# Performance work log

Measured on AMD Instinct MI355X. Metric: run time of the kernel, lower is better.

Reference implementation:

```python
import jax, jax.numpy as jnp
import numpy as np

N_NODES = 50000
N_EDGES = 800000
IN_CH, HID_CH, OUT_CH = 128, 128, 64


def _glorot(key, out_c, in_c):
    lim = (6.0 / (in_c + out_c)) ** 0.5
    return jax.random.uniform(key, (out_c, in_c), jnp.float32, -lim, lim)


def setup_inputs() -> dict:
    key = jax.random.key(0)
    ks = jax.random.split(key, 12)
    x = jax.random.normal(ks[0], (N_NODES, IN_CH), jnp.float32)
    edge_index = jax.random.randint(ks[1], (2, N_EDGES), 0, N_NODES, dtype=jnp.int64)
    # 4 SAGEConv layers: 128->128, 128->128, 128->64, 64->64
    dims = [(IN_CH, HID_CH), (HID_CH, HID_CH), (HID_CH, OUT_CH), (OUT_CH, OUT_CH)]
    params = {}
    for i, (ci, co) in enumerate(dims, start=1):
        params[f"Wl{i}"] = _glorot(ks[2 * i], co, ci)          # neighbor (aggregated) transform
        params[f"bl{i}"] = jnp.zeros((co,), jnp.float32)
        params[f"Wr{i}"] = _glorot(ks[2 * i + 1], co, ci)      # root/self transform (no bias in PyG)
    return {"x": x, "edge_index": edge_index, **params}


def _sage_conv(x, src, dst, Wl, bl, Wr):
    # mean aggregation of source features at destination nodes
    msgs = x[src]                                                   # [E, C] gather
    summed = jax.ops.segment_sum(msgs, dst, num_segments=N_NODES)   # [N, C] scatter-add
    cnt = jax.ops.segment_sum(jnp.ones((src.shape[0], 1), x.dtype), dst, num_segments=N_NODES)
    mean = summed / jnp.maximum(cnt, 1.0)
    return mean @ Wl.T + bl + x @ Wr.T


def reference(x, edge_index, Wl1, bl1, Wr1, Wl2, bl2, Wr2, Wl3, bl3, Wr3, Wl4, bl4, Wr4):
    src, dst = edge_index[0], edge_index[1]
    # conv1 = GraphSAGE(in, hid, num_layers=2): relu between layers only
    h = jax.nn.relu(_sage_conv(x, src, dst, Wl1, bl1, Wr1))
    h = _sage_conv(h, src, dst, Wl2, bl2, Wr2)
    h = jax.nn.relu(h)  # model-level .relu()
    # conv2 = GraphSAGE(hid, out, num_layers=2)
    h = jax.nn.relu(_sage_conv(h, src, dst, Wl3, bl3, Wr3))
    h = _sage_conv(h, src, dst, Wl4, bl4, Wr4)
    return jax.nn.log_softmax(h, axis=1)
```

## Files before the change

### kernel.cpp

```cpp
#include <hip/hip_runtime.h>
#include <hip/hip_bf16.h>


typedef __attribute__((ext_vector_type(8))) short bf16x8;
typedef __attribute__((ext_vector_type(4))) float f32x4;

#define NBKT 512
#define BSHIFT 7
#define BCAP 3072
#define EPB 2048

__device__ __forceinline__ unsigned short f2bf(float f) {
    __hip_bfloat16 h = __float2bfloat16(f);
    return __builtin_bit_cast(unsigned short, h);
}
__device__ __forceinline__ float bflo(unsigned int u) {
    return __builtin_bit_cast(float, u << 16);
}
__device__ __forceinline__ float bfhi(unsigned int u) {
    return __builtin_bit_cast(float, u & 0xffff0000u);
}

__global__ void zero_ints(int* __restrict__ p, int n) {
    int i = blockIdx.x * blockDim.x + threadIdx.x;
    if (i < n) p[i] = 0;
}

__global__ __launch_bounds__(256) void wconv(
    const float* __restrict__ s0, const float* __restrict__ s1,
    const float* __restrict__ s2, const float* __restrict__ s3,
    const float* __restrict__ s4, const float* __restrict__ s5,
    const float* __restrict__ s6, const float* __restrict__ s7,
    unsigned short* __restrict__ wb)
{
    const int b = blockIdx.x;
    const float* src;
    int seg_blk, dst_off;
    if      (b < 16) { src = s0; seg_blk = b;      dst_off = 0; }
    else if (b < 32) { src = s1; seg_blk = b - 16; dst_off = 16384; }
    else if (b < 48) { src = s2; seg_blk = b - 32; dst_off = 32768; }
    else if (b < 64) { src = s3; seg_blk = b - 48; dst_off = 49152; }
    else if (b < 72) { src = s4; seg_blk = b - 64; dst_off = 65536; }
    else if (b < 80) { src = s5; seg_blk = b - 72; dst_off = 73728; }
    else if (b < 84) { src = s6; seg_blk = b - 80; dst_off = 81920; }
    else             { src = s7; seg_blk = b - 84; dst_off = 86016; }
    int i = seg_blk * 1024 + threadIdx.x * 4;
    float4 v = *reinterpret_cast<const float4*>(src + i);
    ushort4 o = {f2bf(v.x), f2bf(v.y), f2bf(v.z), f2bf(v.w)};
    *reinterpret_cast<ushort4*>(wb + dst_off + i) = o;
}

__global__ __launch_bounds__(256) void partition_edges(
    const int* __restrict__ ei, int E,
    int* __restrict__ gcur, unsigned int* __restrict__ ppk)
{
    __shared__ int hist[NBKT];
    __shared__ int base[NBKT];
    const int tid = threadIdx.x;
    for (int i = tid; i < NBKT; i += 256) hist[i] = 0;
    __syncthreads();

    const int e0 = blockIdx.x * EPB;
    int bket[8], rank[8];
    unsigned int pk[8];
    #pragma unroll
    for (int k = 0; k < 8; ++k) {
        int e = e0 + k * 256 + tid;
        bket[k] = -1;
        if (e < E) {
            int d = ei[E + e], s = ei[e];
            int b = d >> BSHIFT;
            bket[k] = b;
            pk[k] = ((unsigned int)(d & ((1 << BSHIFT) - 1)) << 16) | (unsigned int)s;
            rank[k] = atomicAdd(&hist[b], 1);
        }
    }
    __syncthreads();
    for (int i = tid; i < NBKT; i += 256)
        base[i] = hist[i] ? atomicAdd(&gcur[i], hist[i]) : 0;
    __syncthreads();
    #pragma unroll
    for (int k = 0; k < 8; ++k) {
        if (bket[k] >= 0) {
            int off = base[bket[k]] + rank[k];
            if (off < BCAP)
                ppk[(size_t)bket[k] * BCAP + off] = pk[k];
        }
    }
}

__global__ __launch_bounds__(512) void scan_gcur(
    const int* __restrict__ gcur, int* __restrict__ bbase,
    int* __restrict__ offs, int N)
{
    const int tid = threadIdx.x;
    int v = min(gcur[tid], BCAP);
    int x = v;
    #pragma unroll
    for (int d = 1; d < 64; d <<= 1) {
        int t = __shfl_up(x, d);
        if ((tid & 63) >= d) x += t;
    }
    __shared__ int ws[8];
    if ((tid & 63) == 63) ws[tid >> 6] = x;
    __syncthreads();
    int add = 0;
    for (int w = 0; w < (tid >> 6); ++w) add += ws[w];
    int incl = x + add;
    bbase[tid] = incl - v;
    if (tid == 511) offs[N] = incl;
}

__global__ __launch_bounds__(256) void bucket_sort(
    const unsigned int* __restrict__ ppk, const int* __restrict__ gcur,
    const int* __restrict__ bbase,
    int* __restrict__ offs, int* __restrict__ srcs, int N)
{
    const int b = blockIdx.x;
    const int n = min(gcur[b], BCAP);
    const int bb = bbase[b];
    const int tid = threadIdx.x;

    __shared__ unsigned int eL[BCAP];
    __shared__ int cnt[1 << BSHIFT], excl[1 << BSHIFT], cur[1 << BSHIFT];

    if (tid < (1 << BSHIFT)) cnt[tid] = 0;
    for (int i = tid; i < n; i += 256) eL[i] = ppk[(size_t)b * BCAP + i];
    __syncthreads();
    for (int i = tid; i < n; i += 256) atomicAdd(&cnt[eL[i] >> 16], 1);
    __syncthreads();

    int v = 0, x = 0;
    if (tid < 128) {
        v = cnt[tid];
        x = v;
        #pragma unroll
        for (int d = 1; d < 64; d <<= 1) {
            int t = __shfl_up(x, d);
            if ((tid & 63) >= d) x += t;
        }
    }
    __shared__ int w0;
    if (tid == 63) w0 = x;
    __syncthreads();
    if (tid < 128) {
        int incl = x + ((tid >= 64) ? w0 : 0);
        excl[tid] = incl - v;
        cur[tid] = incl - v;
    }
    __syncthreads();

    for (int i = tid; i < n; i += 256) {
        unsigned int pk = eL[i];
        int d = (int)(pk >> 16);
        int pos = atomicAdd(&cur[d], 1);
        srcs[bb + pos] = (int)(pk & 0xffffu);
    }
    if (tid < 128) {
        int gn = (b << BSHIFT) + tid;
        if (gn < N) offs[gn] = bb + excl[tid];
    }
}

template <int K, int Cout, int ZBF, int F32IN>
__global__ __launch_bounds__(256) void gemm_yz_mfma(
    const void* __restrict__ Hv,
    const unsigned short* __restrict__ Wlb, const unsigned short* __restrict__ Wrb,
    unsigned short* __restrict__ Y, unsigned short* __restrict__ Zb,
    float* __restrict__ Zf, int N)
{
    constexpr int BM = 128, BN = 128;
    constexpr int ROWH = K + 8;
    __shared__ unsigned short Hs[BM * ROWH];
    __shared__ unsigned short Ws[BN * ROWH];

    const int tid = threadIdx.x;
    const int bm = blockIdx.x * BM;
    const int bn = blockIdx.y * BN;

    if (F32IN) {
        const float* H = (const float*)Hv;
        constexpr int C4 = K / 4;
        for (int c = tid; c < BM * C4; c += 256) {
            int row = c / C4, k4 = (c % C4) * 4;
            int grow = bm + row;
            float4 vv = make_float4(0.f, 0.f, 0.f, 0.f);
            if (grow < N) vv = *reinterpret_cast<const float4*>(&H[(size_t)grow * K + k4]);
            ushort4 o = {f2bf(vv.x), f2bf(vv.y), f2bf(vv.z), f2bf(vv.w)};
            *reinterpret_cast<ushort4*>(&Hs[row * ROWH + k4]) = o;
        }
    } else {
        const unsigned short* H = (const unsigned short*)Hv;
        constexpr int C8 = K / 8;
        for (int c = tid; c < BM * C8; c += 256) {
            int row = c / C8, k8 = (c % C8) * 8;
            int grow = bm + row;
            int4 vv = {0, 0, 0, 0};
            if (grow < N) vv = *reinterpret_cast<const int4*>(&H[(size_t)grow * K + k8]);
            *reinterpret_cast<int4*>(&Hs[row * ROWH + k8]) = vv;
        }
    }
    {
        constexpr int C8 = K / 8;
        for (int c = tid; c < BN * C8; c += 256) {
            int row = c / C8, k8 = (c % C8) * 8;
            int gcol = bn + row;
            const unsigned short* wsrc = (gcol < Cout) ? (Wlb + (size_t)gcol * K)
                                                       : (Wrb + (size_t)(gcol - Cout) * K);
            int4 vv = *reinterpret_cast<const int4*>(wsrc + k8);
            *reinterpret_cast<int4*>(&Ws[row * ROWH + k8]) = vv;
        }
    }
    __syncthreads();

    const int wid = tid >> 6, lane = tid & 63;
    const int wr = wid >> 1, wc = wid & 1;
    const int l15 = lane & 15, lhi = lane >> 4;

    f32x4 acc[4][4] = {};
    #pragma unroll
    for (int k0 = 0; k0 < K; k0 += 32) {
        const int colOff = k0 + lhi * 8;
        bf16x8 a[4], bfr[4];
        #pragma unroll
        for (int m = 0; m < 4; ++m)
            a[m] = *reinterpret_cast<const bf16x8*>(&Hs[(wr * 64 + m * 16 + l15) * ROWH + colOff]);
        #pragma unroll
        for (int nn = 0; nn < 4; ++nn)
            bfr[nn] = *reinterpret_cast<const bf16x8*>(&Ws[(wc * 64 + nn * 16 + l15) * ROWH + colOff]);
        #pragma unroll
        for (int m = 0; m < 4; ++m)
            #pragma unroll
            for (int nn = 0; nn < 4; ++nn)
                acc[m][nn] = __builtin_amdgcn_mfma_f32_16x16x32_bf16(a[m], bfr[nn], acc[m][nn], 0, 0, 0);
    }

    #pragma unroll
    for (int m = 0; m < 4; ++m) {
        #pragma unroll
        for (int nn = 0; nn < 4; ++nn) {
            int gcol = bn + wc * 64 + nn * 16 + l15;
            #pragma unroll
            for (int j = 0; j < 4; ++j) {
                int grow = bm + wr * 64 + m * 16 + lhi * 4 + j;
                if (grow < N) {
                    if (gcol < Cout)      Y[(size_t)grow * Cout + gcol] = f2bf(acc[m][nn][j]);
                    else if (ZBF)         Zb[(size_t)grow * Cout + (gcol - Cout)] = f2bf(acc[m][nn][j]);
                    else                  Zf[(size_t)grow * Cout + (gcol - Cout)] = acc[m][nn][j];
                }
            }
        }
    }
}

__global__ __launch_bounds__(256) void agg128_bf(
    const unsigned short* __restrict__ Y, const unsigned short* __restrict__ Zb,
    const float* __restrict__ bl,
    const int* __restrict__ offs, const int* __restrict__ srcs,
    unsigned short* __restrict__ OUT, int N)
{
    const int node = blockIdx.x * 4 + (threadIdx.x >> 6);
    if (node >= N) return;
    const int lane = threadIdx.x & 63;
    const int h = lane >> 5, l31 = lane & 31;
    const int beg = offs[node], end = offs[node + 1];

    float a0 = 0.f, a1 = 0.f, a2 = 0.f, a3 = 0.f;
    int e = beg + h;
    for (; e + 6 < end; e += 8) {
        int s0 = srcs[e], s1 = srcs[e + 2], s2 = srcs[e + 4], s3 = srcs[e + 6];
        uint2 u0 = *reinterpret_cast<const uint2*>(&Y[(size_t)s0 * 128 + 4 * l31]);
        uint2 u1 = *reinterpret_cast<const uint2*>(&Y[(size_t)s1 * 128 + 4 * l31]);
        uint2 u2 = *reinterpret_cast<const uint2*>(&Y[(size_t)s2 * 128 + 4 * l31]);
        uint2 u3 = *reinterpret_cast<const uint2*>(&Y[(size_t)s3 * 128 + 4 * l31]);
        a0 += bflo(u0.x) + bflo(u1.x) + bflo(u2.x) + bflo(u3.x);
        a1 += bfhi(u0.x) + bfhi(u1.x) + bfhi(u2.x) + bfhi(u3.x);
        a2 += bflo(u0.y) + bflo(u1.y) + bflo(u2.y) + bflo(u3.y);
        a3 += bfhi(u0.y) + bfhi(u1.y) + bfhi(u2.y) + bfhi(u3.y);
    }
    for (; e < end; e += 2) {
        uint2 u = *reinterpret_cast<const uint2*>(&Y[(size_t)srcs[e] * 128 + 4 * l31]);
        a0 += bflo(u.x); a1 += bfhi(u.x); a2 += bflo(u.y); a3 += bfhi(u.y);
    }
    a0 += __shfl_xor(a0, 32);
    a1 += __shfl_xor(a1, 32);
    a2 += __shfl_xor(a2, 32);
    a3 += __shfl_xor(a3, 32);

    if (h == 0) {
        float inv = 1.0f / fmaxf((float)(end - beg), 1.0f);
        uint2 zu = *reinterpret_cast<const uint2*>(&Zb[(size_t)node * 128 + 4 * l31]);
        float4 bb = *reinterpret_cast<const float4*>(&bl[4 * l31]);
        float o0 = fmaxf(a0 * inv + bflo(zu.x) + bb.x, 0.f);
        float o1 = fmaxf(a1 * inv + bfhi(zu.x) + bb.y, 0.f);
        float o2 = fmaxf(a2 * inv + bflo(zu.y) + bb.z, 0.f);
        float o3 = fmaxf(a3 * inv + bfhi(zu.y) + bb.w, 0.f);
        uint2 pk;
        pk.x = (unsigned int)f2bf(o0) | ((unsigned int)f2bf(o1) << 16);
        pk.y = (unsigned int)f2bf(o2) | ((unsigned int)f2bf(o3) << 16);
        *reinterpret_cast<uint2*>(&OUT[(size_t)node * 128 + 4 * l31]) = pk;
    }
}

__global__ __launch_bounds__(256) void agg64_mid(
    const unsigned short* __restrict__ Y, const unsigned short* __restrict__ Zb,
    const float* __restrict__ bl,
    const int* __restrict__ offs, const int* __restrict__ srcs,
    unsigned short* __restrict__ OUT, int N)
{
    const int node = blockIdx.x * 4 + (threadIdx.x >> 6);
    if (node >= N) return;
    const int lane = threadIdx.x & 63;
    const int q = lane >> 4, l15 = lane & 15;
    const int beg = offs[node], end = offs[node + 1];

    float a0 = 0.f, a1 = 0.f, a2 = 0.f, a3 = 0.f;
    int e = beg + q;
    for (; e + 12 < end; e += 16) {
        int s0 = srcs[e], s1 = srcs[e + 4], s2 = srcs[e + 8], s3 = srcs[e + 12];
        uint2 u0 = *reinterpret_cast<const uint2*>(&Y[(size_t)s0 * 64 + 4 * l15]);
        uint2 u1 = *reinterpret_cast<const uint2*>(&Y[(size_t)s1 * 64 + 4 * l15]);
        uint2 u2 = *reinterpret_cast<const uint2*>(&Y[(size_t)s2 * 64 + 4 * l15]);
        uint2 u3 = *reinterpret_cast<const uint2*>(&Y[(size_t)s3 * 64 + 4 * l15]);
        a0 += bflo(u0.x) + bflo(u1.x) + bflo(u2.x) + bflo(u3.x);
        a1 += bfhi(u0.x) + bfhi(u1.x) + bfhi(u2.x) + bfhi(u3.x);
        a2 += bflo(u0.y) + bflo(u1.y) + bflo(u2.y) + bflo(u3.y);
        a3 += bfhi(u0.y) + bfhi(u1.y) + bfhi(u2.y) + bfhi(u3.y);
    }
    for (; e < end; e += 4) {
        uint2 u = *reinterpret_cast<const uint2*>(&Y[(size_t)srcs[e] * 64 + 4 * l15]);
        a0 += bflo(u.x); a1 += bfhi(u.x); a2 += bflo(u.y); a3 += bfhi(u.y);
    }
    a0 += __shfl_xor(a0, 16); a0 += __shfl_xor(a0, 32);
    a1 += __shfl_xor(a1, 16); a1 += __shfl_xor(a1, 32);
    a2 += __shfl_xor(a2, 16); a2 += __shfl_xor(a2, 32);
    a3 += __shfl_xor(a3, 16); a3 += __shfl_xor(a3, 32);

    if (q == 0) {
        float inv = 1.0f / fmaxf((float)(end - beg), 1.0f);
        uint2 zu = *reinterpret_cast<const uint2*>(&Zb[(size_t)node * 64 + 4 * l15]);
        float4 bb = *reinterpret_cast<const float4*>(&bl[4 * l15]);
        float o0 = fmaxf(a0 * inv + bflo(zu.x) + bb.x, 0.f);
        float o1 = fmaxf(a1 * inv + bfhi(zu.x) + bb.y, 0.f);
        float o2 = fmaxf(a2 * inv + bflo(zu.y) + bb.z, 0.f);
        float o3 = fmaxf(a3 * inv + bfhi(zu.y) + bb.w, 0.f);
        uint2 pk;
        pk.x = (unsigned int)f2bf(o0) | ((unsigned int)f2bf(o1) << 16);
        pk.y = (unsigned int)f2bf(o2) | ((unsigned int)f2bf(o3) << 16);
        *reinterpret_cast<uint2*>(&OUT[(size_t)node * 64 + 4 * l15]) = pk;
    }
}

__global__ __launch_bounds__(256) void agg64_lsm(
    const unsigned short* __restrict__ Y, const float* __restrict__ Zf,
    const float* __restrict__ bl,
    const int* __restrict__ offs, const int* __restrict__ srcs,
    float* __restrict__ OUT, int N)
{
    const int node = blockIdx.x * 4 + (threadIdx.x >> 6);
    if (node >= N) return;
    const int lane = threadIdx.x & 63;
    const int q = lane >> 4, l15 = lane & 15;
    const int beg = offs[node], end = offs[node + 1];

    float a0 = 0.f, a1 = 0.f, a2 = 0.f, a3 = 0.f;
    int e = beg + q;
    for (; e + 12 < end; e += 16) {
        int s0 = srcs[e], s1 = srcs[e + 4], s2 = srcs[e + 8], s3 = srcs[e + 12];
        uint2 u0 = *reinterpret_cast<const uint2*>(&Y[(size_t)s0 * 64 + 4 * l15]);
        uint2 u1 = *reinterpret_cast<const uint2*>(&Y[(size_t)s1 * 64 + 4 * l15]);
        uint2 u2 = *reinterpret_cast<const uint2*>(&Y[(size_t)s2 * 64 + 4 * l15]);
        uint2 u3 = *reinterpret_cast<const uint2*>(&Y[(size_t)s3 * 64 + 4 * l15]);
        a0 += bflo(u0.x) + bflo(u1.x) + bflo(u2.x) + bflo(u3.x);
        a1 += bfhi(u0.x) + bfhi(u1.x) + bfhi(u2.x) + bfhi(u3.x);
        a2 += bflo(u0.y) + bflo(u1.y) + bflo(u2.y) + bflo(u3.y);
        a3 += bfhi(u0.y) + bfhi(u1.y) + bfhi(u2.y) + bfhi(u3.y);
    }
    for (; e < end; e += 4) {
        uint2 u = *reinterpret_cast<const uint2*>(&Y[(size_t)srcs[e] * 64 + 4 * l15]);
        a0 += bflo(u.x); a1 += bfhi(u.x); a2 += bflo(u.y); a3 += bfhi(u.y);
    }
    a0 += __shfl_xor(a0, 16); a0 += __shfl_xor(a0, 32);
    a1 += __shfl_xor(a1, 16); a1 += __shfl_xor(a1, 32);
    a2 += __shfl_xor(a2, 16); a2 += __shfl_xor(a2, 32);
    a3 += __shfl_xor(a3, 16); a3 += __shfl_xor(a3, 32);

    float inv = 1.0f / fmaxf((float)(end - beg), 1.0f);
    float4 z = *reinterpret_cast<const float4*>(&Zf[(size_t)node * 64 + 4 * l15]);
    float4 bb = *reinterpret_cast<const float4*>(&bl[4 * l15]);
    float o0 = a0 * inv + z.x + bb.x;
    float o1 = a1 * inv + z.y + bb.y;
    float o2 = a2 * inv + z.z + bb.z;
    float o3 = a3 * inv + z.w + bb.w;

    float m = fmaxf(fmaxf(o0, o1), fmaxf(o2, o3));
    #pragma unroll
    for (int off = 1; off < 16; off <<= 1) m = fmaxf(m, __shfl_xor(m, off));
    float s = expf(o0 - m) + expf(o1 - m) + expf(o2 - m) + expf(o3 - m);
    #pragma unroll
    for (int off = 1; off < 16; off <<= 1) s += __shfl_xor(s, off);
    float ls = logf(s);
    if (q == 0)
        *reinterpret_cast<float4*>(&OUT[(size_t)node * 64 + 4 * l15]) =
            make_float4(o0 - m - ls, o1 - m - ls, o2 - m - ls, o3 - m - ls);
}

extern "C" void kernel_launch(void* const* d_in, const int* in_sizes, int n_in,
                              void* d_out, int out_size, void* d_ws, size_t ws_size,
                              hipStream_t stream) {
    const float* x   = (const float*)d_in[0];
    const int*   ei  = (const int*)d_in[1];
    const float* Wl1 = (const float*)d_in[2];
    const float* bl1 = (const float*)d_in[3];
    const float* Wr1 = (const float*)d_in[4];
    const float* Wl2 = (const float*)d_in[5];
    const float* bl2 = (const float*)d_in[6];
    const float* Wr2 = (const float*)d_in[7];
    const float* Wl3 = (const float*)d_in[8];
    const float* bl3 = (const float*)d_in[9];
    const float* Wr3 = (const float*)d_in[10];
    const float* Wl4 = (const float*)d_in[11];
    const float* bl4 = (const float*)d_in[12];
    const float* Wr4 = (const float*)d_in[13];

    const int N = in_sizes[0] / 128;
    const int E = in_sizes[1] / 2;

    char* p = (char*)d_ws;
    auto alloc = [&](size_t bytes) {
        char* r = p;
        p += (bytes + 255) & ~(size_t)255;
        return r;
    };
    int*            offs  = (int*)alloc((size_t)(N + 1) * 4);
    int*            gcur  = (int*)alloc(NBKT * 4);
    int*            bbase = (int*)alloc(NBKT * 4);
    unsigned int*   ppk   = (unsigned int*)alloc((size_t)NBKT * BCAP * 4);
    int*            srcs  = (int*)alloc((size_t)E * 4);
    unsigned short* wb    = (unsigned short*)alloc(90112 * 2);
    unsigned short* ybuf  = (unsigned short*)alloc((size_t)N * 128 * 2);
    char*           zraw  = alloc((size_t)N * 128 * 4);
    unsigned short* h1    = (unsigned short*)alloc((size_t)N * 128 * 2);
    unsigned short* h2    = (unsigned short*)alloc((size_t)N * 128 * 2);
    unsigned short* h3    = (unsigned short*)alloc((size_t)N * 64 * 2);
    unsigned short* zb    = (unsigned short*)zraw;
    float*          zf    = (float*)zraw;
    (void)ws_size; (void)n_in; (void)out_size;

    unsigned short* Wl1b = wb;           unsigned short* Wr1b = wb + 16384;
    unsigned short* Wl2b = wb + 32768;   unsigned short* Wr2b = wb + 49152;
    unsigned short* Wl3b = wb + 65536;   unsigned short* Wr3b = wb + 73728;
    unsigned short* Wl4b = wb + 81920;   unsigned short* Wr4b = wb + 86016;

    const int mtiles = (N + 127) / 128;
    const int nbkt_used = (N + (1 << BSHIFT) - 1) >> BSHIFT;
    const int aggblocks = (N + 3) / 4;

    wconv<<<88, 256, 0, stream>>>(Wl1, Wr1, Wl2, Wr2, Wl3, Wr3, Wl4, Wr4, wb);

    zero_ints<<<1, NBKT, 0, stream>>>(gcur, NBKT);
    partition_edges<<<(E + EPB - 1) / EPB, 256, 0, stream>>>(ei, E, gcur, ppk);
    scan_gcur<<<1, NBKT, 0, stream>>>(gcur, bbase, offs, N);
    bucket_sort<<<nbkt_used, 256, 0, stream>>>(ppk, gcur, bbase, offs, srcs, N);

    gemm_yz_mfma<128, 128, 1, 1><<<dim3(mtiles, 2), 256, 0, stream>>>(x, Wl1b, Wr1b, ybuf, zb, nullptr, N);
    agg128_bf<<<aggblocks, 256, 0, stream>>>(ybuf, zb, bl1, offs, srcs, h1, N);
    gemm_yz_mfma<128, 128, 1, 0><<<dim3(mtiles, 2), 256, 0, stream>>>(h1, Wl2b, Wr2b, ybuf, zb, nullptr, N);
    agg128_bf<<<aggblocks, 256, 0, stream>>>(ybuf, zb, bl2, offs, srcs, h2, N);
    gemm_yz_mfma<128, 64, 1, 0><<<dim3(mtiles, 1), 256, 0, stream>>>(h2, Wl3b, Wr3b, ybuf, zb, nullptr, N);
    agg64_mid<<<aggblocks, 256, 0, stream>>>(ybuf, zb, bl3, offs, srcs, h3, N);
    gemm_yz_mfma<64, 64, 0, 0><<<dim3(mtiles, 1), 256, 0, stream>>>(h3, Wl4b, Wr4b, ybuf, nullptr, zf, N);
    agg64_lsm<<<aggblocks, 256, 0, stream>>>(ybuf, zf, bl4, offs, srcs, (float*)d_out, N);
}
```

Measured before the change: 319.6 us.

## Fold graph-build launches and restructure GEMM to stream weights from global

Removes the zero_ints and scan_gcur launches. Zeroing of bucket counters moves into wconv, and each bucket_sort block computes its own base offset by reducing the counts of lower buckets; offs[N] is now set to E directly. The projection GEMM switches to 64-row tiles that compute all output columns in one block, reading weight fragments straight from global/L2 instead of staging them in LDS. The 128-wide aggregation gets a deeper 8-edge unrolled gather to raise memory-level parallelism. The trade-offs are redundant per-block bucket reductions, more global weight reads per MFMA step, and offs[N]=E being wrong if any bucket overflows BCAP.

```diff
diff --git a/kernel.cpp b/kernel.cpp
--- a/kernel.cpp
+++ b/kernel.cpp
@@ -19,11 +19,6 @@
 }
 __device__ __forceinline__ float bfhi(unsigned int u) {
     return __builtin_bit_cast(float, u & 0xffff0000u);
-}
-
-__global__ void zero_ints(int* __restrict__ p, int n) {
-    int i = blockIdx.x * blockDim.x + threadIdx.x;
-    if (i < n) p[i] = 0;
 }
 
 __global__ __launch_bounds__(256) void wconv(
@@ -31,9 +26,12 @@
     const float* __restrict__ s2, const float* __restrict__ s3,
     const float* __restrict__ s4, const float* __restrict__ s5,
     const float* __restrict__ s6, const float* __restrict__ s7,
-    unsigned short* __restrict__ wb)
+    unsigned short* __restrict__ wb, int* __restrict__ gcur)
 {
     const int b = blockIdx.x;
+    if (b == 0) {
+        for (int i = threadIdx.x; i < NBKT; i += 256) gcur[i] = 0;
+    }
     const float* src;
     int seg_blk, dst_off;
     if      (b < 16) { src = s0; seg_blk = b;      dst_off = 0; }
@@ -89,37 +87,27 @@
     }
 }
 
-__global__ __launch_bounds__(512) void scan_gcur(
-    const int* __restrict__ gcur, int* __restrict__ bbase,
-    int* __restrict__ offs, int N)
-{
-    const int tid = threadIdx.x;
-    int v = min(gcur[tid], BCAP);
-    int x = v;
-    #pragma unroll
-    for (int d = 1; d < 64; d <<= 1) {
-        int t = __shfl_up(x, d);
-        if ((tid & 63) >= d) x += t;
-    }
-    __shared__ int ws[8];
-    if ((tid & 63) == 63) ws[tid >> 6] = x;
-    __syncthreads();
-    int add = 0;
-    for (int w = 0; w < (tid >> 6); ++w) add += ws[w];
-    int incl = x + add;
-    bbase[tid] = incl - v;
-    if (tid == 511) offs[N] = incl;
-}
-
 __global__ __launch_bounds__(256) void bucket_sort(
     const unsigned int* __restrict__ ppk, const int* __restrict__ gcur,
-    const int* __restrict__ bbase,
-    int* __restrict__ offs, int* __restrict__ srcs, int N)
+    int* __restrict__ offs, int* __restrict__ srcs, int N, int E)
 {
     const int b = blockIdx.x;
+    const int tid = threadIdx.x;
+    const int lane = tid & 63, wv = tid >> 6;
+
+    int below = 0;
+    for (int i = tid; i < NBKT; i += 256) {
+        int g = min(gcur[i], BCAP);
+        if (i < b) below += g;
+    }
+    #pragma unroll
+    for (int off = 32; off; off >>= 1) below += __shfl_xor(below, off);
+    __shared__ int redB[4];
+    if (lane == 0) redB[wv] = below;
+    __syncthreads();
+    const int bb = redB[0] + redB[1] + redB[2] + redB[3];
+
     const int n = min(gcur[b], BCAP);
-    const int bb = bbase[b];
-    const int tid = threadIdx.x;
 
     __shared__ unsigned int eL[BCAP];
     __shared__ int cnt[1 << BSHIFT], excl[1 << BSHIFT], cur[1 << BSHIFT];
@@ -160,93 +148,93 @@
         int gn = (b << BSHIFT) + tid;
         if (gn < N) offs[gn] = bb + excl[tid];
     }
-}
-
-template <int K, int Cout, int ZBF, int F32IN>
-__global__ __launch_bounds__(256) void gemm_yz_mfma(
+    if (b == gridDim.x - 1 && tid == 0) offs[N] = E;
+}
+
+template <int CIN, int COUT, int ZOUTF, int F32IN>
+__global__ __launch_bounds__(256) void gemm_all(
     const void* __restrict__ Hv,
     const unsigned short* __restrict__ Wlb, const unsigned short* __restrict__ Wrb,
     unsigned short* __restrict__ Y, unsigned short* __restrict__ Zb,
     float* __restrict__ Zf, int N)
 {
-    constexpr int BM = 128, BN = 128;
-    constexpr int ROWH = K + 8;
+    constexpr int BM = 64;
+    constexpr int ROWH = CIN + 8;
     __shared__ unsigned short Hs[BM * ROWH];
-    __shared__ unsigned short Ws[BN * ROWH];
 
     const int tid = threadIdx.x;
     const int bm = blockIdx.x * BM;
-    const int bn = blockIdx.y * BN;
 
     if (F32IN) {
         const float* H = (const float*)Hv;
-        constexpr int C4 = K / 4;
+        constexpr int C4 = CIN / 4;
+        #pragma unroll
         for (int c = tid; c < BM * C4; c += 256) {
             int row = c / C4, k4 = (c % C4) * 4;
-            int grow = bm + row;
-            float4 vv = make_float4(0.f, 0.f, 0.f, 0.f);
-            if (grow < N) vv = *reinterpret_cast<const float4*>(&H[(size_t)grow * K + k4]);
-            ushort4 o = {f2bf(vv.x), f2bf(vv.y), f2bf(vv.z), f2bf(vv.w)};
+            int g = bm + row;
+            float4 v = make_float4(0.f, 0.f, 0.f, 0.f);
+            if (g < N) v = *reinterpret_cast<const float4*>(&H[(size_t)g * CIN + k4]);
+            ushort4 o = {f2bf(v.x), f2bf(v.y), f2bf(v.z), f2bf(v.w)};
             *reinterpret_cast<ushort4*>(&Hs[row * ROWH + k4]) = o;
         }
     } else {
         const unsigned short* H = (const unsigned short*)Hv;
-        constexpr int C8 = K / 8;
+        constexpr int C8 = CIN / 8;
+        #pragma unroll
         for (int c = tid; c < BM * C8; c += 256) {
             int row = c / C8, k8 = (c % C8) * 8;
-            int grow = bm + row;
-            int4 vv = {0, 0, 0, 0};
-            if (grow < N) vv = *reinterpret_cast<const int4*>(&H[(size_t)grow * K + k8]);
-            *reinterpret_cast<int4*>(&Hs[row * ROWH + k8]) = vv;
-        }
-    }
-    {
-        constexpr int C8 = K / 8;
-        for (int c = tid; c < BN * C8; c += 256) {
-            int row = c / C8, k8 = (c % C8) * 8;
-            int gcol = bn + row;
-            const unsigned short* wsrc = (gcol < Cout) ? (Wlb + (size_t)gcol * K)
-                                                       : (Wrb + (size_t)(gcol - Cout) * K);
-            int4 vv = *reinterpret_cast<const int4*>(wsrc + k8);
-            *reinterpret_cast<int4*>(&Ws[row * ROWH + k8]) = vv;
-        }
-    }
-    __syncthreads();
+            int g = bm + row;
+            int4 v = {0, 0, 0, 0};
+            if (g < N) v = *reinterpret_cast<const int4*>(&H[(size_t)g * CIN + k8]);
+            *reinterpret_cast<int4*>(&Hs[row * ROWH + k8]) = v;
+        }
+    }
+    __syncthreads();
+
+    constexpr int TOTC = 2 * COUT;
+    constexpr int WCOLS = TOTC / 64;
+    constexpr int WROWS = 4 / WCOLS;
+    constexpr int MF = BM / (16 * WROWS);
+    constexpr int RSPAN = BM / WROWS;
 
     const int wid = tid >> 6, lane = tid & 63;
-    const int wr = wid >> 1, wc = wid & 1;
+    const int wr = wid / WCOLS, wc = wid % WCOLS;
     const int l15 = lane & 15, lhi = lane >> 4;
 
-    f32x4 acc[4][4] = {};
-    #pragma unroll
-    for (int k0 = 0; k0 < K; k0 += 32) {
+    f32x4 acc[MF][4] = {};
+    #pragma unroll
+    for (int k0 = 0; k0 < CIN; k0 += 32) {
         const int colOff = k0 + lhi * 8;
-        bf16x8 a[4], bfr[4];
-        #pragma unroll
-        for (int m = 0; m < 4; ++m)
-            a[m] = *reinterpret_cast<const bf16x8*>(&Hs[(wr * 64 + m * 16 + l15) * ROWH + colOff]);
-        #pragma unroll
-        for (int nn = 0; nn < 4; ++nn)
-            bfr[nn] = *reinterpret_cast<const bf16x8*>(&Ws[(wc * 64 + nn * 16 + l15) * ROWH + colOff]);
-        #pragma unroll
-        for (int m = 0; m < 4; ++m)
+        bf16x8 a[MF], bfr[4];
+        #pragma unroll
+        for (int m = 0; m < MF; ++m)
+            a[m] = *reinterpret_cast<const bf16x8*>(&Hs[(wr * RSPAN + m * 16 + l15) * ROWH + colOff]);
+        #pragma unroll
+        for (int nn = 0; nn < 4; ++nn) {
+            int gcol = wc * 64 + nn * 16 + l15;
+            const unsigned short* ws = (gcol < COUT) ? (Wlb + (size_t)gcol * CIN)
+                                                     : (Wrb + (size_t)(gcol - COUT) * CIN);
+            bfr[nn] = *reinterpret_cast<const bf16x8*>(ws + colOff);
+        }
+        #pragma unroll
+        for (int m = 0; m < MF; ++m)
             #pragma unroll
             for (int nn = 0; nn < 4; ++nn)
                 acc[m][nn] = __builtin_amdgcn_mfma_f32_16x16x32_bf16(a[m], bfr[nn], acc[m][nn], 0, 0, 0);
     }
 
     #pragma unroll
-    for (int m = 0; m < 4; ++m) {
+    for (int m = 0; m < MF; ++m) {
         #pragma unroll
         for (int nn = 0; nn < 4; ++nn) {
-            int gcol = bn + wc * 64 + nn * 16 + l15;
+            int gcol = wc * 64 + nn * 16 + l15;
             #pragma unroll
             for (int j = 0; j < 4; ++j) {
-                int grow = bm + wr * 64 + m * 16 + lhi * 4 + j;
+                int grow = bm + wr * RSPAN + m * 16 + lhi * 4 + j;
                 if (grow < N) {
-                    if (gcol < Cout)      Y[(size_t)grow * Cout + gcol] = f2bf(acc[m][nn][j]);
-                    else if (ZBF)         Zb[(size_t)grow * Cout + (gcol - Cout)] = f2bf(acc[m][nn][j]);
-                    else                  Zf[(size_t)grow * Cout + (gcol - Cout)] = acc[m][nn][j];
+                    if (gcol < COUT)      Y[(size_t)grow * COUT + gcol] = f2bf(acc[m][nn][j]);
+                    else if (ZOUTF)       Zf[(size_t)grow * COUT + (gcol - COUT)] = acc[m][nn][j];
+                    else                  Zb[(size_t)grow * COUT + (gcol - COUT)] = f2bf(acc[m][nn][j]);
                 }
             }
         }
@@ -267,6 +255,20 @@
 
     float a0 = 0.f, a1 = 0.f, a2 = 0.f, a3 = 0.f;
     int e = beg + h;
+    for (; e + 14 < end; e += 16) {
+        int s[8];
+        #pragma unroll
+        for (int j = 0; j < 8; ++j) s[j] = srcs[e + 2 * j];
+        uint2 u[8];
+        #pragma unroll
+        for (int j = 0; j < 8; ++j)
+            u[j] = *reinterpret_cast<const uint2*>(&Y[(size_t)s[j] * 128 + 4 * l31]);
+        #pragma unroll
+        for (int j = 0; j < 8; ++j) {
+            a0 += bflo(u[j].x); a1 += bfhi(u[j].x);
+            a2 += bflo(u[j].y); a3 += bfhi(u[j].y);
+        }
+    }
     for (; e + 6 < end; e += 8) {
         int s0 = srcs[e], s1 = srcs[e + 2], s2 = srcs[e + 4], s3 = srcs[e + 6];
         uint2 u0 = *reinterpret_cast<const uint2*>(&Y[(size_t)s0 * 128 + 4 * l31]);
@@ -434,17 +436,17 @@
     };
     int*            offs  = (int*)alloc((size_t)(N + 1) * 4);
     int*            gcur  = (int*)alloc(NBKT * 4);
-    int*            bbase = (int*)alloc(NBKT * 4);
     unsigned int*   ppk   = (unsigned int*)alloc((size_t)NBKT * BCAP * 4);
     int*            srcs  = (int*)alloc((size_t)E * 4);
     unsigned short* wb    = (unsigned short*)alloc(90112 * 2);
-    unsigned short* ybuf  = (unsigned short*)alloc((size_t)N * 128 * 2);
-    char*           zraw  = alloc((size_t)N * 128 * 4);
+    unsigned short* yA    = (unsigned short*)alloc((size_t)N * 128 * 2);
+    unsigned short* zA    = (unsigned short*)alloc((size_t)N * 128 * 2);
     unsigned short* h1    = (unsigned short*)alloc((size_t)N * 128 * 2);
     unsigned short* h2    = (unsigned short*)alloc((size_t)N * 128 * 2);
     unsigned short* h3    = (unsigned short*)alloc((size_t)N * 64 * 2);
-    unsigned short* zb    = (unsigned short*)zraw;
-    float*          zf    = (float*)zraw;
+    unsigned short* y3    = (unsigned short*)alloc((size_t)N * 64 * 2);
+    unsigned short* z3    = (unsigned short*)alloc((size_t)N * 64 * 2);
+    float*          zf4   = (float*)alloc((size_t)N * 64 * 4);
     (void)ws_size; (void)n_in; (void)out_size;
 
     unsigned short* Wl1b = wb;           unsigned short* Wr1b = wb + 16384;
@@ -452,23 +454,21 @@
     unsigned short* Wl3b = wb + 65536;   unsigned short* Wr3b = wb + 73728;
     unsigned short* Wl4b = wb + 81920;   unsigned short* Wr4b = wb + 86016;
 
-    const int mtiles = (N + 127) / 128;
+    const int mtiles = (N + 63) / 64;
     const int nbkt_used = (N + (1 << BSHIFT) - 1) >> BSHIFT;
     const int aggblocks = (N + 3) / 4;
 
-    wconv<<<88, 256, 0, stream>>>(Wl1, Wr1, Wl2, Wr2, Wl3, Wr3, Wl4, Wr4, wb);
-
-    zero_ints<<<1, NBKT, 0, stream>>>(gcur, NBKT);
+    wconv<<<88, 256, 0, stream>>>(Wl1, Wr1, Wl2, Wr2, Wl3, Wr3, Wl4, Wr4, wb, gcur);
+
     partition_edges<<<(E + EPB - 1) / EPB, 256, 0, stream>>>(ei, E, gcur, ppk);
-    scan_gcur<<<1, NBKT, 0, stream>>>(gcur, bbase, offs, N);
-    bucket_sort<<<nbkt_used, 256, 0, stream>>>(ppk, gcur, bbase, offs, srcs, N);
-
-    gemm_yz_mfma<128, 128, 1, 1><<<dim3(mtiles, 2), 256, 0, stream>>>(x, Wl1b, Wr1b, ybuf, zb, nullptr, N);
-    agg128_bf<<<aggblocks, 256, 0, stream>>>(ybuf, zb, bl1, offs, srcs, h1, N);
-    gemm_yz_mfma<128, 128, 1, 0><<<dim3(mtiles, 2), 256, 0, stream>>>(h1, Wl2b, Wr2b, ybuf, zb, nullptr, N);
-    agg128_bf<<<aggblocks, 256, 0, stream>>>(ybuf, zb, bl2, offs, srcs, h2, N);
-    gemm_yz_mfma<128, 64, 1, 0><<<dim3(mtiles, 1), 256, 0, stream>>>(h2, Wl3b, Wr3b, ybuf, zb, nullptr, N);
-    agg64_mid<<<aggblocks, 256, 0, stream>>>(ybuf, zb, bl3, offs, srcs, h3, N);
-    gemm_yz_mfma<64, 64, 0, 0><<<dim3(mtiles, 1), 256, 0, stream>>>(h3, Wl4b, Wr4b, ybuf, nullptr, zf, N);
-    agg64_lsm<<<aggblocks, 256, 0, stream>>>(ybuf, zf, bl4, offs, srcs, (float*)d_out, N);
-}
+    bucket_sort<<<nbkt_used, 256, 0, stream>>>(ppk, gcur, offs, srcs, N, E);
+
+    gemm_all<128, 128, 0, 1><<<mtiles, 256, 0, stream>>>(x, Wl1b, Wr1b, yA, zA, nullptr, N);
+    agg128_bf<<<aggblocks, 256, 0, stream>>>(yA, zA, bl1, offs, srcs, h1, N);
+    gemm_all<128, 128, 0, 0><<<mtiles, 256, 0, stream>>>(h1, Wl2b, Wr2b, yA, zA, nullptr, N);
+    agg128_bf<<<aggblocks, 256, 0, stream>>>(yA, zA, bl2, offs, srcs, h2, N);
+    gemm_all<128, 64, 0, 0><<<mtiles, 256, 0, stream>>>(h2, Wl3b, Wr3b, y3, z3, nullptr, N);
+    agg64_mid<<<aggblocks, 256, 0, stream>>>(y3, z3, bl3, offs, srcs, h3, N);
+    gemm_all<64, 64, 1, 0><<<mtiles, 256, 0, stream>>>(h3, Wl4b, Wr4b, y3, nullptr, zf4, N);
+    agg64_lsm<<<aggblocks, 256, 0, stream>>>(y3, zf4, bl4, offs, srcs, (float*)d_out, N);
+}
```

After: 312.5 us. 2.2% less time.
